# Optimization experiments

Hardware: AMD Instinct MI355X
Metric: run time of the kernel (lower is better)

## Reference

```python
import jax, jax.numpy as jnp
import numpy as np

DIM = 384
HEADS = 12
W = 7  # window_size
N = W * W
B = 4096

def _relative_position_index(ws):
    ch = np.arange(ws)
    coords = np.stack(np.meshgrid(ch, ch, indexing='ij'))  # [2, W, W]
    cf = coords.reshape(2, -1)  # [2, W*W]
    rel = cf[:, :, None] - cf[:, None, :]  # [2, N, N]
    rel = rel.transpose(1, 2, 0)
    rel[:, :, 0] += ws - 1
    rel[:, :, 1] += ws - 1
    rel[:, :, 0] *= 2 * ws - 1
    return rel.sum(-1).astype(np.int32)  # [N, N]

def setup_inputs() -> dict:
    key = jax.random.key(0)
    ks = jax.random.split(key, 8)
    s = 0.02
    return {
        'x': jax.random.normal(ks[0], (B, N, DIM), jnp.float32),
        'y': jax.random.normal(ks[1], (B, N, DIM), jnp.float32),
        'q_w': jax.random.normal(ks[2], (DIM, DIM), jnp.float32) * s,
        'q_b': jnp.zeros((DIM,), jnp.float32),
        'kv_w': jax.random.normal(ks[3], (2 * DIM, DIM), jnp.float32) * s,
        'kv_b': jnp.zeros((2 * DIM,), jnp.float32),
        'proj_w': jax.random.normal(ks[4], (DIM, DIM), jnp.float32) * s,
        'proj_b': jnp.zeros((DIM,), jnp.float32),
        'rel_table': jax.random.normal(ks[5], ((2 * W - 1) ** 2, HEADS), jnp.float32) * s,
        'rel_index': jnp.asarray(_relative_position_index(W)),
    }

def reference(x, y, q_w, q_b, kv_w, kv_b, proj_w, proj_b, rel_table, rel_index):
    Bx, N1, C = x.shape
    N2 = y.shape[1]
    hd = C // HEADS
    scale = hd ** -0.5
    # projections (torch Linear: x @ W^T + b)
    q = (x @ q_w.T + q_b).reshape(Bx, N1, HEADS, hd)
    kv = (y @ kv_w.T + kv_b).reshape(Bx, N2, 2, HEADS, hd)
    k = kv[:, :, 0]  # [B, N2, H, d]
    v = kv[:, :, 1]
    attn = jnp.einsum('bqhd,bkhd->bhqk', q, k) * scale
    # relative position bias: [N1, N2, H] -> [H, N1, N2]
    bias = rel_table[rel_index.reshape(-1)].reshape(N1, N2, HEADS)
    attn = attn + jnp.transpose(bias, (2, 0, 1))[None]
    attn = jax.nn.softmax(attn, axis=-1)
    out = jnp.einsum('bhqk,bkhd->bqhd', attn, v).reshape(Bx, N1, C)
    return out @ proj_w.T + proj_b
```

## Files before the change

### kernel.cpp

```cpp
#include <hip/hip_runtime.h>

#define DIM 384
#define HEADS 12
#define HD 32
#define NTOK 49
#define NWIN 4096
#define MTOT (NWIN*NTOK)
#define PSTR 72

typedef __attribute__((ext_vector_type(8))) __bf16 bf16x8;
typedef __attribute__((ext_vector_type(4))) __bf16 bf16x4;
typedef __attribute__((ext_vector_type(4))) float f32x4;

static __device__ __forceinline__ f32x4 mfma16(bf16x8 a, bf16x8 b, f32x4 c) {
  return __builtin_amdgcn_mfma_f32_16x16x32_bf16(a, b, c, 0, 0, 0);
}

static __device__ __forceinline__ void gload_lds16(const void* g, void* l) {
  __builtin_amdgcn_global_load_lds(
      (const __attribute__((address_space(1))) unsigned int*)g,
      (__attribute__((address_space(3))) unsigned int*)l, 16, 0, 0);
}

static __device__ __forceinline__ bf16x4 cvt4(float4 v) {
  bf16x4 t;
  t[0]=(__bf16)v.x; t[1]=(__bf16)v.y; t[2]=(__bf16)v.z; t[3]=(__bf16)v.w;
  return t;
}

__global__ void k_prep(const float* __restrict__ qw, const float* __restrict__ kvw,
                       const float* __restrict__ pw, const float* __restrict__ rel_table,
                       const int* __restrict__ rel_index,
                       __bf16* __restrict__ qw_bf, __bf16* __restrict__ kvw_bf,
                       __bf16* __restrict__ pw_bf, float* __restrict__ bias_pad) {
  int i = blockIdx.x * 256 + threadIdx.x;
  if (i < DIM*DIM)   qw_bf[i] = (__bf16)qw[i];
  if (i < 2*DIM*DIM) kvw_bf[i] = (__bf16)kvw[i];
  if (i < DIM*DIM)   pw_bf[i] = (__bf16)pw[i];
  if (i < HEADS*64*64) {
    int h = i >> 12, rem = i & 4095, q = rem >> 6, k = rem & 63;
    float v;
    if (k >= NTOK)      v = -1e30f;
    else if (q >= NTOK) v = 0.0f;
    else v = rel_table[rel_index[q*NTOK + k] * HEADS + h];
    bias_pad[i] = v;
  }
}

__global__ __launch_bounds__(256, 4) void k_qkv(
    const float* __restrict__ x, const float* __restrict__ y,
    const __bf16* __restrict__ qw_bf, const __bf16* __restrict__ kvw_bf,
    const float* __restrict__ q_b, const float* __restrict__ kv_b,
    __bf16* __restrict__ Qws, __bf16* __restrict__ Kws, __bf16* __restrict__ Vws)
{
  int b = blockIdx.x;
  int orig = (b & 7) * 1764 + (b >> 3);
  int mtile = orig / 9;
  int nt9 = orig - mtile*9;
  const float* A; const __bf16* Bw; const float* bias; __bf16* Cout;
  int wrow0, col0;
  if (nt9 < 3) { A = x; Bw = qw_bf; bias = q_b; Cout = Qws; wrow0 = nt9*128; col0 = wrow0; }
  else {
    A = y; Bw = kvw_bf; bias = kv_b; wrow0 = (nt9-3)*128;
    if (wrow0 < DIM) { Cout = Kws; col0 = wrow0; } else { Cout = Vws; col0 = wrow0 - DIM; }
  }
  bias += wrow0;

  __shared__ __align__(16) __bf16 As[2*128*32];
  __shared__ __align__(16) __bf16 Bs[3*128*32];

  int t = threadIdx.x, lane = t & 63, wave = t >> 6;
  int l15 = lane & 15, g = lane >> 4;
  int wr = (wave >> 1) * 64, wc = (wave & 1) * 64;
  int row0b = mtile*128;

  int c8 = lane & 7;
  int r8 = lane >> 3;
  int swk = (lane >> 4) & 3;
  const float* asrc = A + (size_t)(row0b + wave*32 + r8)*DIM + c8*4;
  unsigned lwb = (unsigned)wave*2048 + (unsigned)r8*64
               + ((((c8 >> 1) ^ swk) << 4) + (c8 & 1)*8);

  int sr  = 2*(lane >> 3) + ((lane >> 2) & 1);
  int scb = (lane & 3) ^ ((lane >> 3) & 3);
  const __bf16* bsrc0 = Bw + (size_t)(wrow0 + (wave*2    )*16 + sr)*DIM + scb*8;
  const __bf16* bsrc1 = Bw + (size_t)(wrow0 + (wave*2 + 1)*16 + sr)*DIM + scb*8;

  f32x4 acc[4][4];
  #pragma unroll
  for (int a=0;a<4;a++)
    #pragma unroll
    for (int bb=0;bb<4;bb++) acc[a][bb] = (f32x4){0.f,0.f,0.f,0.f};

  {
    float4 s0 = *(const float4*)(asrc);
    float4 s1 = *(const float4*)(asrc +  8*DIM);
    float4 s2 = *(const float4*)(asrc + 16*DIM);
    float4 s3 = *(const float4*)(asrc + 24*DIM);
    gload_lds16(bsrc0,      (char*)Bs +        (wave*2  )*1024);
    gload_lds16(bsrc1,      (char*)Bs +        (wave*2+1)*1024);
    gload_lds16(bsrc0 + 32, (char*)Bs + 8192 + (wave*2  )*1024);
    gload_lds16(bsrc1 + 32, (char*)Bs + 8192 + (wave*2+1)*1024);
    *(bf16x4*)((char*)As + lwb +    0) = cvt4(s0);
    *(bf16x4*)((char*)As + lwb +  512) = cvt4(s1);
    *(bf16x4*)((char*)As + lwb + 1024) = cvt4(s2);
    *(bf16x4*)((char*)As + lwb + 1536) = cvt4(s3);
    asm volatile("s_waitcnt vmcnt(2)" ::: "memory");
    asm volatile("s_waitcnt lgkmcnt(0)" ::: "memory");
    __builtin_amdgcn_s_barrier();
  }

  int lslot = l15*64 + ((g ^ ((l15 >> 1) & 3)) << 4);

  #pragma unroll
  for (int kt = 0; kt < 12; ++kt) {
    const int cur2 = kt & 1, nxt2 = cur2 ^ 1;
    const int cur3 = kt % 3, pre3 = (kt + 2) % 3;
    float4 s0, s1, s2, s3;
    if (kt < 11) {
      int kk = (kt + 1) * 32;
      s0 = *(const float4*)(asrc + kk);
      s1 = *(const float4*)(asrc + kk +  8*DIM);
      s2 = *(const float4*)(asrc + kk + 16*DIM);
      s3 = *(const float4*)(asrc + kk + 24*DIM);
    }
    if (kt < 10) {
      int kk = (kt + 2) * 32;
      gload_lds16(bsrc0 + kk, (char*)Bs + pre3*8192 + (wave*2  )*1024);
      gload_lds16(bsrc1 + kk, (char*)Bs + pre3*8192 + (wave*2+1)*1024);
    }
    bf16x8 af[4], bfv[4];
    #pragma unroll
    for (int a=0;a<4;a++)
      af[a]  = *(const bf16x8*)((const char*)As + cur2*8192 + (wr + a*16)*64 + lslot);
    #pragma unroll
    for (int bb=0;bb<4;bb++)
      bfv[bb] = *(const bf16x8*)((const char*)Bs + cur3*8192 + (wc + bb*16)*64 + lslot);
    #pragma unroll
    for (int a=0;a<4;a++)
      #pragma unroll
      for (int bb=0;bb<4;bb++)
        acc[a][bb] = mfma16(af[a], bfv[bb], acc[a][bb]);
    if (kt < 11) {
      *(bf16x4*)((char*)As + nxt2*8192 + lwb +    0) = cvt4(s0);
      *(bf16x4*)((char*)As + nxt2*8192 + lwb +  512) = cvt4(s1);
      *(bf16x4*)((char*)As + nxt2*8192 + lwb + 1024) = cvt4(s2);
      *(bf16x4*)((char*)As + nxt2*8192 + lwb + 1536) = cvt4(s3);
      if (kt < 10) asm volatile("s_waitcnt vmcnt(2)" ::: "memory");
      else         asm volatile("s_waitcnt vmcnt(0)" ::: "memory");
      asm volatile("s_waitcnt lgkmcnt(0)" ::: "memory");
      __builtin_amdgcn_s_barrier();
    }
  }

  #pragma unroll
  for (int a=0;a<4;a++) {
    #pragma unroll
    for (int bb=0;bb<4;bb++) {
      int colw = wc + bb*16 + l15;
      float bi = bias[colw];
      size_t cbase = (size_t)(row0b + wr + a*16 + 4*g)*DIM + (col0 + colw);
      #pragma unroll
      for (int r=0;r<4;r++)
        Cout[cbase + (size_t)r*DIM] = (__bf16)(acc[a][bb][r] + bi);
    }
  }
}

__global__ __launch_bounds__(256) void k_attn(
    __bf16* qao,
    const __bf16* __restrict__ Kws, const __bf16* __restrict__ Vws,
    const float* __restrict__ bias_pad)
{
  __shared__ __align__(16) __bf16 Psh[4][64*PSTR];
  __shared__ __align__(16) __bf16 VTsh[4][32*PSTR];
  int b = blockIdx.x;
  int lane = threadIdx.x & 63, wave = threadIdx.x >> 6;
  int l15 = lane & 15, g = lane >> 4;
  __bf16* Pw  = Psh[wave];
  __bf16* VTw = VTsh[wave];
  size_t rowbase = (size_t)b * NTOK * DIM;
  const float scale = 0.17677669529663687f;

  for (int e = lane; e < 32*15; e += 64) {
    int d = e / 15, k = 49 + (e - d*15);
    VTw[d*PSTR + k] = (__bf16)0.0f;
  }

  for (int hh = 0; hh < 3; hh++) {
    int h = wave + hh*4;
    for (int e = lane; e < NTOK*HD; e += 64) {
      int k = e >> 5, d = e & 31;
      VTw[d*PSTR + k] = Vws[rowbase + (size_t)k*DIM + h*HD + d];
    }
    bf16x8 qf[4], kf[4];
    #pragma unroll
    for (int mt=0; mt<4; mt++) {
      int q = 16*mt + l15; if (q > 48) q = 48;
      qf[mt] = *(const bf16x8*)(qao + rowbase + (size_t)q*DIM + h*HD + g*8);
    }
    #pragma unroll
    for (int nt=0; nt<4; nt++) {
      int kk = 16*nt + l15; if (kk > 48) kk = 48;
      kf[nt] = *(const bf16x8*)(Kws + rowbase + (size_t)kk*DIM + h*HD + g*8);
    }
    f32x4 sacc[4][4];
    #pragma unroll
    for (int mt=0; mt<4; mt++)
      #pragma unroll
      for (int nt=0; nt<4; nt++)
        sacc[mt][nt] = mfma16(qf[mt], kf[nt], (f32x4){0.f,0.f,0.f,0.f});

    const float* bt = bias_pad + h*4096;
    float rs[4][4];
    #pragma unroll
    for (int mt=0; mt<4; mt++) {
      #pragma unroll
      for (int r=0; r<4; r++) {
        int q = 16*mt + 4*g + r;
        float v0 = sacc[mt][0][r]*scale + bt[q*64 +  0 + l15];
        float v1 = sacc[mt][1][r]*scale + bt[q*64 + 16 + l15];
        float v2 = sacc[mt][2][r]*scale + bt[q*64 + 32 + l15];
        float v3 = sacc[mt][3][r]*scale + bt[q*64 + 48 + l15];
        float m = fmaxf(fmaxf(v0,v1), fmaxf(v2,v3));
        #pragma unroll
        for (int off=1; off<16; off<<=1) m = fmaxf(m, __shfl_xor(m, off));
        v0 = __expf(v0-m); v1 = __expf(v1-m); v2 = __expf(v2-m); v3 = __expf(v3-m);
        float s = v0+v1+v2+v3;
        #pragma unroll
        for (int off=1; off<16; off<<=1) s += __shfl_xor(s, off);
        rs[mt][r] = s;
        Pw[q*PSTR +  0 + l15] = (__bf16)v0;
        Pw[q*PSTR + 16 + l15] = (__bf16)v1;
        Pw[q*PSTR + 32 + l15] = (__bf16)v2;
        Pw[q*PSTR + 48 + l15] = (__bf16)v3;
      }
    }

    #pragma unroll
    for (int mt=0; mt<4; mt++) {
      #pragma unroll
      for (int dt=0; dt<2; dt++) {
        f32x4 o = (f32x4){0.f,0.f,0.f,0.f};
        #pragma unroll
        for (int ks=0; ks<2; ks++) {
          bf16x8 pa = *(const bf16x8*)(Pw  + (16*mt + l15)*PSTR + 32*ks + 8*g);
          bf16x8 vb = *(const bf16x8*)(VTw + (16*dt + l15)*PSTR + 32*ks + 8*g);
          o = mfma16(pa, vb, o);
        }
        #pragma unroll
        for (int r=0; r<4; r++) {
          int q = 16*mt + 4*g + r;
          if (q < NTOK)
            qao[rowbase + (size_t)q*DIM + h*HD + 16*dt + l15] = (__bf16)(o[r] / rs[mt][r]);
        }
      }
    }
  }
}

__global__ __launch_bounds__(256, 4) void k_proj(
    const __bf16* __restrict__ Aao, const __bf16* __restrict__ pw_bf,
    const float* __restrict__ pb, float* __restrict__ out)
{
  int b = blockIdx.x;
  int orig = (b & 7) * 588 + (b >> 3);
  int mtile = orig / 3;
  int nt = orig - mtile*3;
  int lane = threadIdx.x & 63, wave = threadIdx.x >> 6;
  int l15 = lane & 15, g = lane >> 4;
  int wr = (wave >> 1) * 64, wc = (wave & 1) * 64;
  int row0b = mtile*128;
  int col00 = nt*128;

  __shared__ __align__(16) __bf16 As[3*128*32];
  __shared__ __align__(16) __bf16 Bs[3*128*32];

  int sr  = 2*(lane >> 3) + ((lane >> 2) & 1);
  int scb = (lane & 3) ^ ((lane >> 3) & 3);
  const __bf16* asrc0 = Aao   + (size_t)(row0b + (wave*2    )*16 + sr)*DIM + scb*8;
  const __bf16* asrc1 = Aao   + (size_t)(row0b + (wave*2 + 1)*16 + sr)*DIM + scb*8;
  const __bf16* bsrc0 = pw_bf + (size_t)(col00 + (wave*2    )*16 + sr)*DIM + scb*8;
  const __bf16* bsrc1 = pw_bf + (size_t)(col00 + (wave*2 + 1)*16 + sr)*DIM + scb*8;

  f32x4 acc[4][4];
  #pragma unroll
  for (int a=0;a<4;a++)
    #pragma unroll
    for (int bb=0;bb<4;bb++) acc[a][bb] = (f32x4){0.f,0.f,0.f,0.f};

  {
    gload_lds16(asrc0,      (char*)As +        (wave*2  )*1024);
    gload_lds16(asrc1,      (char*)As +        (wave*2+1)*1024);
    gload_lds16(bsrc0,      (char*)Bs +        (wave*2  )*1024);
    gload_lds16(bsrc1,      (char*)Bs +        (wave*2+1)*1024);
    gload_lds16(asrc0 + 32, (char*)As + 8192 + (wave*2  )*1024);
    gload_lds16(asrc1 + 32, (char*)As + 8192 + (wave*2+1)*1024);
    gload_lds16(bsrc0 + 32, (char*)Bs + 8192 + (wave*2  )*1024);
    gload_lds16(bsrc1 + 32, (char*)Bs + 8192 + (wave*2+1)*1024);
    asm volatile("s_waitcnt vmcnt(4)" ::: "memory");
    __builtin_amdgcn_s_barrier();
  }

  int lslot = l15*64 + ((g ^ ((l15 >> 1) & 3)) << 4);

  #pragma unroll
  for (int kt = 0; kt < 12; ++kt) {
    const int cur3 = kt % 3, pre3 = (kt + 2) % 3;
    if (kt < 10) {
      int kk = (kt + 2) * 32;
      gload_lds16(asrc0 + kk, (char*)As + pre3*8192 + (wave*2  )*1024);
      gload_lds16(asrc1 + kk, (char*)As + pre3*8192 + (wave*2+1)*1024);
      gload_lds16(bsrc0 + kk, (char*)Bs + pre3*8192 + (wave*2  )*1024);
      gload_lds16(bsrc1 + kk, (char*)Bs + pre3*8192 + (wave*2+1)*1024);
    }
    bf16x8 af[4], bfv[4];
    #pragma unroll
    for (int a=0;a<4;a++)
      af[a]  = *(const bf16x8*)((const char*)As + cur3*8192 + (wr + a*16)*64 + lslot);
    #pragma unroll
    for (int bb=0;bb<4;bb++)
      bfv[bb] = *(const bf16x8*)((const char*)Bs + cur3*8192 + (wc + bb*16)*64 + lslot);
    #pragma unroll
    for (int a=0;a<4;a++)
      #pragma unroll
      for (int bb=0;bb<4;bb++)
        acc[a][bb] = mfma16(af[a], bfv[bb], acc[a][bb]);
    if (kt < 11) {
      if (kt < 10) asm volatile("s_waitcnt vmcnt(4)" ::: "memory");
      else         asm volatile("s_waitcnt vmcnt(0)" ::: "memory");
      __builtin_amdgcn_s_barrier();
    }
  }

  #pragma unroll
  for (int a=0;a<4;a++) {
    #pragma unroll
    for (int bb=0;bb<4;bb++) {
      int col = col00 + wc + bb*16 + l15;
      float bi = pb[col];
      size_t cbase = (size_t)(row0b + wr + a*16 + 4*g)*DIM + col;
      #pragma unroll
      for (int r=0;r<4;r++)
        out[cbase + (size_t)r*DIM] = acc[a][bb][r] + bi;
    }
  }
}

extern "C" void kernel_launch(void* const* d_in, const int* in_sizes, int n_in,
                              void* d_out, int out_size, void* d_ws, size_t ws_size,
                              hipStream_t stream)
{
  const float* x   = (const float*)d_in[0];
  const float* y   = (const float*)d_in[1];
  const float* qw  = (const float*)d_in[2];
  const float* qb  = (const float*)d_in[3];
  const float* kvw = (const float*)d_in[4];
  const float* kvb = (const float*)d_in[5];
  const float* pw  = (const float*)d_in[6];
  const float* pb  = (const float*)d_in[7];
  const float* rt  = (const float*)d_in[8];
  const int*   ri  = (const int*)d_in[9];
  float* out = (float*)d_out;

  char* ws = (char*)d_ws;
  const size_t WS_NEEDED = 1376256ull + 3ull*154140672ull;
  if (ws_size < WS_NEEDED) return;

  __bf16* qw_bf    = (__bf16*)(ws);
  __bf16* kvw_bf   = (__bf16*)(ws + 294912);
  __bf16* pw_bf    = (__bf16*)(ws + 884736);
  float*  bias_pad = (float*)(ws + 1179648);
  __bf16* Qws      = (__bf16*)(ws + 1376256);
  __bf16* Kws      = Qws + (size_t)MTOT*DIM;
  __bf16* Vws      = Kws + (size_t)MTOT*DIM;

  k_prep<<<dim3(1152), dim3(256), 0, stream>>>(qw, kvw, pw, rt, ri, qw_bf, kvw_bf, pw_bf, bias_pad);
  k_qkv <<<dim3(1568*9), dim3(256), 0, stream>>>(x, y, qw_bf, kvw_bf, qb, kvb, Qws, Kws, Vws);
  k_attn<<<dim3(NWIN), dim3(256), 0, stream>>>(Qws, Kws, Vws, bias_pad);
  k_proj<<<dim3(1568*3), dim3(256), 0, stream>>>(Qws, pw_bf, pb, out);
}
```

Before: 840.8 us.

## Keep full-K activation row panel in LDS and sweep all output columns

```diff
diff --git a/kernel.cpp b/kernel.cpp
--- a/kernel.cpp
+++ b/kernel.cpp
@@ -47,122 +47,111 @@
   }
 }
 
-__global__ __launch_bounds__(256, 4) void k_qkv(
+__global__ __launch_bounds__(256, 2) void k_qkv2(
     const float* __restrict__ x, const float* __restrict__ y,
     const __bf16* __restrict__ qw_bf, const __bf16* __restrict__ kvw_bf,
     const float* __restrict__ q_b, const float* __restrict__ kv_b,
     __bf16* __restrict__ Qws, __bf16* __restrict__ Kws, __bf16* __restrict__ Vws)
 {
-  int b = blockIdx.x;
-  int orig = (b & 7) * 1764 + (b >> 3);
-  int mtile = orig / 9;
-  int nt9 = orig - mtile*9;
-  const float* A; const __bf16* Bw; const float* bias; __bf16* Cout;
-  int wrow0, col0;
-  if (nt9 < 3) { A = x; Bw = qw_bf; bias = q_b; Cout = Qws; wrow0 = nt9*128; col0 = wrow0; }
-  else {
-    A = y; Bw = kvw_bf; bias = kv_b; wrow0 = (nt9-3)*128;
-    if (wrow0 < DIM) { Cout = Kws; col0 = wrow0; } else { Cout = Vws; col0 = wrow0 - DIM; }
-  }
-  bias += wrow0;
-
-  __shared__ __align__(16) __bf16 As[2*128*32];
+  __shared__ __align__(16) __bf16 Asub[12*64*32];
   __shared__ __align__(16) __bf16 Bs[3*128*32];
 
-  int t = threadIdx.x, lane = t & 63, wave = t >> 6;
-  int l15 = lane & 15, g = lane >> 4;
-  int wr = (wave >> 1) * 64, wc = (wave & 1) * 64;
-  int row0b = mtile*128;
-
-  int c8 = lane & 7;
-  int r8 = lane >> 3;
-  int swk = (lane >> 4) & 3;
-  const float* asrc = A + (size_t)(row0b + wave*32 + r8)*DIM + c8*4;
-  unsigned lwb = (unsigned)wave*2048 + (unsigned)r8*64
-               + ((((c8 >> 1) ^ swk) << 4) + (c8 & 1)*8);
-
-  int sr  = 2*(lane >> 3) + ((lane >> 2) & 1);
-  int scb = (lane & 3) ^ ((lane >> 3) & 3);
-  const __bf16* bsrc0 = Bw + (size_t)(wrow0 + (wave*2    )*16 + sr)*DIM + scb*8;
-  const __bf16* bsrc1 = Bw + (size_t)(wrow0 + (wave*2 + 1)*16 + sr)*DIM + scb*8;
-
-  f32x4 acc[4][4];
-  #pragma unroll
-  for (int a=0;a<4;a++)
-    #pragma unroll
-    for (int bb=0;bb<4;bb++) acc[a][bb] = (f32x4){0.f,0.f,0.f,0.f};
+  const int b = blockIdx.x;
+  const int type = b & 1;
+  const int mtile = b >> 1;
+  const float* A = type ? y : x;
+  const __bf16* Bw = type ? kvw_bf : qw_bf;
+  const int NCH = type ? 6 : 3;
+  const int row0b = mtile * 64;
+
+  const int t = threadIdx.x, lane = t & 63, wave = t >> 6;
+  const int l15 = lane & 15, g = lane >> 4;
+  const int wm = wave >> 1, wn = wave & 1;
 
   {
-    float4 s0 = *(const float4*)(asrc);
-    float4 s1 = *(const float4*)(asrc +  8*DIM);
-    float4 s2 = *(const float4*)(asrc + 16*DIM);
-    float4 s3 = *(const float4*)(asrc + 24*DIM);
-    gload_lds16(bsrc0,      (char*)Bs +        (wave*2  )*1024);
-    gload_lds16(bsrc1,      (char*)Bs +        (wave*2+1)*1024);
-    gload_lds16(bsrc0 + 32, (char*)Bs + 8192 + (wave*2  )*1024);
-    gload_lds16(bsrc1 + 32, (char*)Bs + 8192 + (wave*2+1)*1024);
-    *(bf16x4*)((char*)As + lwb +    0) = cvt4(s0);
-    *(bf16x4*)((char*)As + lwb +  512) = cvt4(s1);
-    *(bf16x4*)((char*)As + lwb + 1024) = cvt4(s2);
-    *(bf16x4*)((char*)As + lwb + 1536) = cvt4(s3);
-    asm volatile("s_waitcnt vmcnt(2)" ::: "memory");
-    asm volatile("s_waitcnt lgkmcnt(0)" ::: "memory");
-    __builtin_amdgcn_s_barrier();
-  }
-
-  int lslot = l15*64 + ((g ^ ((l15 >> 1) & 3)) << 4);
-
-  #pragma unroll
-  for (int kt = 0; kt < 12; ++kt) {
-    const int cur2 = kt & 1, nxt2 = cur2 ^ 1;
-    const int cur3 = kt % 3, pre3 = (kt + 2) % 3;
-    float4 s0, s1, s2, s3;
-    if (kt < 11) {
-      int kk = (kt + 1) * 32;
-      s0 = *(const float4*)(asrc + kk);
-      s1 = *(const float4*)(asrc + kk +  8*DIM);
-      s2 = *(const float4*)(asrc + kk + 16*DIM);
-      s3 = *(const float4*)(asrc + kk + 24*DIM);
-    }
-    if (kt < 10) {
-      int kk = (kt + 2) * 32;
-      gload_lds16(bsrc0 + kk, (char*)Bs + pre3*8192 + (wave*2  )*1024);
-      gload_lds16(bsrc1 + kk, (char*)Bs + pre3*8192 + (wave*2+1)*1024);
-    }
-    bf16x8 af[4], bfv[4];
-    #pragma unroll
-    for (int a=0;a<4;a++)
-      af[a]  = *(const bf16x8*)((const char*)As + cur2*8192 + (wr + a*16)*64 + lslot);
-    #pragma unroll
-    for (int bb=0;bb<4;bb++)
-      bfv[bb] = *(const bf16x8*)((const char*)Bs + cur3*8192 + (wc + bb*16)*64 + lslot);
-    #pragma unroll
-    for (int a=0;a<4;a++)
+    const int c8 = lane & 7, r8 = lane >> 3;
+    const int swk = (lane >> 4) & 3;
+    const float* asrc = A + (size_t)(row0b + wave*8 + r8)*DIM + c8*4;
+    const unsigned lwA = (unsigned)(wave*8 + r8)*64
+                       + ((((c8 >> 1) ^ swk) << 4) + (c8 & 1)*8);
+    #pragma unroll
+    for (int st = 0; st < 12; ++st) {
+      float4 u0 = *(const float4*)(asrc + st*32);
+      float4 u1 = *(const float4*)(asrc + st*32 + 32*DIM);
+      *(bf16x4*)((char*)Asub + st*4096 + lwA)        = cvt4(u0);
+      *(bf16x4*)((char*)Asub + st*4096 + 2048 + lwA) = cvt4(u1);
+    }
+  }
+
+  const int sr  = 2*(lane >> 3) + ((lane >> 2) & 1);
+  const int scb = (lane & 3) ^ ((lane >> 3) & 3);
+  const __bf16* bsrc0 = Bw + (size_t)((wave*2    )*16 + sr)*DIM + scb*8;
+  const __bf16* bsrc1 = Bw + (size_t)((wave*2 + 1)*16 + sr)*DIM + scb*8;
+
+  gload_lds16(bsrc0,      (char*)Bs        + (wave*2  )*1024);
+  gload_lds16(bsrc1,      (char*)Bs        + (wave*2+1)*1024);
+  gload_lds16(bsrc0 + 32, (char*)Bs + 8192 + (wave*2  )*1024);
+  gload_lds16(bsrc1 + 32, (char*)Bs + 8192 + (wave*2+1)*1024);
+  asm volatile("s_waitcnt lgkmcnt(0)" ::: "memory");
+  __builtin_amdgcn_s_barrier();
+
+  const int lslot = l15*64 + ((g ^ ((l15 >> 1) & 3)) << 4);
+
+  for (int jn = 0; jn < NCH; ++jn) {
+    const size_t co = (size_t)jn * 49152;
+    const size_t cn = co + 49152;
+    f32x4 acc[2][4];
+    #pragma unroll
+    for (int a=0;a<2;a++)
+      #pragma unroll
+      for (int bb=0;bb<4;bb++) acc[a][bb] = (f32x4){0.f,0.f,0.f,0.f};
+
+    #pragma unroll
+    for (int kt = 0; kt < 12; ++kt) {
+      if (kt == 11 && jn == NCH-1) asm volatile("s_waitcnt vmcnt(0)" ::: "memory");
+      else                         asm volatile("s_waitcnt vmcnt(2)" ::: "memory");
+      __builtin_amdgcn_s_barrier();
+
+      const int cb = kt % 3;
+      bf16x8 af[2], bfv[4];
+      af[0] = *(const bf16x8*)((const char*)Asub + kt*4096 + (wm*32     )*64 + lslot);
+      af[1] = *(const bf16x8*)((const char*)Asub + kt*4096 + (wm*32 + 16)*64 + lslot);
       #pragma unroll
       for (int bb=0;bb<4;bb++)
-        acc[a][bb] = mfma16(af[a], bfv[bb], acc[a][bb]);
-    if (kt < 11) {
-      *(bf16x4*)((char*)As + nxt2*8192 + lwb +    0) = cvt4(s0);
-      *(bf16x4*)((char*)As + nxt2*8192 + lwb +  512) = cvt4(s1);
-      *(bf16x4*)((char*)As + nxt2*8192 + lwb + 1024) = cvt4(s2);
-      *(bf16x4*)((char*)As + nxt2*8192 + lwb + 1536) = cvt4(s3);
-      if (kt < 10) asm volatile("s_waitcnt vmcnt(2)" ::: "memory");
-      else         asm volatile("s_waitcnt vmcnt(0)" ::: "memory");
-      asm volatile("s_waitcnt lgkmcnt(0)" ::: "memory");
-      __builtin_amdgcn_s_barrier();
-    }
-  }
-
-  #pragma unroll
-  for (int a=0;a<4;a++) {
-    #pragma unroll
-    for (int bb=0;bb<4;bb++) {
-      int colw = wc + bb*16 + l15;
-      float bi = bias[colw];
-      size_t cbase = (size_t)(row0b + wr + a*16 + 4*g)*DIM + (col0 + colw);
-      #pragma unroll
-      for (int r=0;r<4;r++)
-        Cout[cbase + (size_t)r*DIM] = (__bf16)(acc[a][bb][r] + bi);
+        bfv[bb] = *(const bf16x8*)((const char*)Bs + cb*8192 + (wn*64 + bb*16)*64 + lslot);
+
+      if (kt < 10) {
+        gload_lds16(bsrc0 + co + (kt+2)*32, (char*)Bs + ((kt+2)%3)*8192 + (wave*2  )*1024);
+        gload_lds16(bsrc1 + co + (kt+2)*32, (char*)Bs + ((kt+2)%3)*8192 + (wave*2+1)*1024);
+      } else if (jn < NCH-1) {
+        const int k2 = kt - 10;
+        gload_lds16(bsrc0 + cn + k2*32, (char*)Bs + ((kt+2)%3)*8192 + (wave*2  )*1024);
+        gload_lds16(bsrc1 + cn + k2*32, (char*)Bs + ((kt+2)%3)*8192 + (wave*2+1)*1024);
+      }
+
+      #pragma unroll
+      for (int a=0;a<2;a++)
+        #pragma unroll
+        for (int bb=0;bb<4;bb++)
+          acc[a][bb] = mfma16(af[a], bfv[bb], acc[a][bb]);
+    }
+
+    const float* biasp = (type ? kv_b : q_b) + jn*128;
+    __bf16* Cout; int col0;
+    if (!type)        { Cout = Qws; col0 = jn*128; }
+    else if (jn < 3)  { Cout = Kws; col0 = jn*128; }
+    else              { Cout = Vws; col0 = (jn-3)*128; }
+    #pragma unroll
+    for (int a=0;a<2;a++) {
+      #pragma unroll
+      for (int bb=0;bb<4;bb++) {
+        const int colw = wn*64 + bb*16 + l15;
+        const float bi = biasp[colw];
+        const size_t cbase = (size_t)(row0b + wm*32 + a*16 + 4*g)*DIM + col0 + colw;
+        #pragma unroll
+        for (int r=0;r<4;r++)
+          Cout[cbase + (size_t)r*DIM] = (__bf16)(acc[a][bb][r] + bi);
+      }
     }
   }
 }
@@ -259,90 +248,98 @@
   }
 }
 
-__global__ __launch_bounds__(256, 4) void k_proj(
+__global__ __launch_bounds__(256, 2) void k_proj2(
     const __bf16* __restrict__ Aao, const __bf16* __restrict__ pw_bf,
     const float* __restrict__ pb, float* __restrict__ out)
 {
-  int b = blockIdx.x;
-  int orig = (b & 7) * 588 + (b >> 3);
-  int mtile = orig / 3;
-  int nt = orig - mtile*3;
-  int lane = threadIdx.x & 63, wave = threadIdx.x >> 6;
-  int l15 = lane & 15, g = lane >> 4;
-  int wr = (wave >> 1) * 64, wc = (wave & 1) * 64;
-  int row0b = mtile*128;
-  int col00 = nt*128;
-
-  __shared__ __align__(16) __bf16 As[3*128*32];
+  __shared__ __align__(16) __bf16 Asub[12*64*32];
   __shared__ __align__(16) __bf16 Bs[3*128*32];
 
-  int sr  = 2*(lane >> 3) + ((lane >> 2) & 1);
-  int scb = (lane & 3) ^ ((lane >> 3) & 3);
-  const __bf16* asrc0 = Aao   + (size_t)(row0b + (wave*2    )*16 + sr)*DIM + scb*8;
-  const __bf16* asrc1 = Aao   + (size_t)(row0b + (wave*2 + 1)*16 + sr)*DIM + scb*8;
-  const __bf16* bsrc0 = pw_bf + (size_t)(col00 + (wave*2    )*16 + sr)*DIM + scb*8;
-  const __bf16* bsrc1 = pw_bf + (size_t)(col00 + (wave*2 + 1)*16 + sr)*DIM + scb*8;
-
-  f32x4 acc[4][4];
-  #pragma unroll
-  for (int a=0;a<4;a++)
-    #pragma unroll
-    for (int bb=0;bb<4;bb++) acc[a][bb] = (f32x4){0.f,0.f,0.f,0.f};
+  const int mtile = blockIdx.x;
+  const int row0b = mtile * 64;
+  const int t = threadIdx.x, lane = t & 63, wave = t >> 6;
+  const int l15 = lane & 15, g = lane >> 4;
+  const int wm = wave >> 1, wn = wave & 1;
+
+  const int sr  = 2*(lane >> 3) + ((lane >> 2) & 1);
+  const int scb = (lane & 3) ^ ((lane >> 3) & 3);
 
   {
-    gload_lds16(asrc0,      (char*)As +        (wave*2  )*1024);
-    gload_lds16(asrc1,      (char*)As +        (wave*2+1)*1024);
-    gload_lds16(bsrc0,      (char*)Bs +        (wave*2  )*1024);
-    gload_lds16(bsrc1,      (char*)Bs +        (wave*2+1)*1024);
-    gload_lds16(asrc0 + 32, (char*)As + 8192 + (wave*2  )*1024);
-    gload_lds16(asrc1 + 32, (char*)As + 8192 + (wave*2+1)*1024);
-    gload_lds16(bsrc0 + 32, (char*)Bs + 8192 + (wave*2  )*1024);
-    gload_lds16(bsrc1 + 32, (char*)Bs + 8192 + (wave*2+1)*1024);
-    asm volatile("s_waitcnt vmcnt(4)" ::: "memory");
-    __builtin_amdgcn_s_barrier();
-  }
-
-  int lslot = l15*64 + ((g ^ ((l15 >> 1) & 3)) << 4);
-
-  #pragma unroll
-  for (int kt = 0; kt < 12; ++kt) {
-    const int cur3 = kt % 3, pre3 = (kt + 2) % 3;
-    if (kt < 10) {
-      int kk = (kt + 2) * 32;
-      gload_lds16(asrc0 + kk, (char*)As + pre3*8192 + (wave*2  )*1024);
-      gload_lds16(asrc1 + kk, (char*)As + pre3*8192 + (wave*2+1)*1024);
-      gload_lds16(bsrc0 + kk, (char*)Bs + pre3*8192 + (wave*2  )*1024);
-      gload_lds16(bsrc1 + kk, (char*)Bs + pre3*8192 + (wave*2+1)*1024);
-    }
-    bf16x8 af[4], bfv[4];
-    #pragma unroll
-    for (int a=0;a<4;a++)
-      af[a]  = *(const bf16x8*)((const char*)As + cur3*8192 + (wr + a*16)*64 + lslot);
-    #pragma unroll
-    for (int bb=0;bb<4;bb++)
-      bfv[bb] = *(const bf16x8*)((const char*)Bs + cur3*8192 + (wc + bb*16)*64 + lslot);
-    #pragma unroll
-    for (int a=0;a<4;a++)
+    const __bf16* aj0 = Aao + (size_t)(row0b +  0 + sr)*DIM + scb*8;
+    const __bf16* aj1 = Aao + (size_t)(row0b + 16 + sr)*DIM + scb*8;
+    const __bf16* aj2 = Aao + (size_t)(row0b + 32 + sr)*DIM + scb*8;
+    const __bf16* aj3 = Aao + (size_t)(row0b + 48 + sr)*DIM + scb*8;
+    #pragma unroll
+    for (int stl = 0; stl < 3; ++stl) {
+      const int st = wave*3 + stl;
+      gload_lds16(aj0 + st*32, (char*)Asub + st*4096 +    0);
+      gload_lds16(aj1 + st*32, (char*)Asub + st*4096 + 1024);
+      gload_lds16(aj2 + st*32, (char*)Asub + st*4096 + 2048);
+      gload_lds16(aj3 + st*32, (char*)Asub + st*4096 + 3072);
+    }
+  }
+
+  const __bf16* bsrc0 = pw_bf + (size_t)((wave*2    )*16 + sr)*DIM + scb*8;
+  const __bf16* bsrc1 = pw_bf + (size_t)((wave*2 + 1)*16 + sr)*DIM + scb*8;
+  gload_lds16(bsrc0,      (char*)Bs        + (wave*2  )*1024);
+  gload_lds16(bsrc1,      (char*)Bs        + (wave*2+1)*1024);
+  gload_lds16(bsrc0 + 32, (char*)Bs + 8192 + (wave*2  )*1024);
+  gload_lds16(bsrc1 + 32, (char*)Bs + 8192 + (wave*2+1)*1024);
+  asm volatile("s_waitcnt vmcnt(4)" ::: "memory");
+  __builtin_amdgcn_s_barrier();
+
+  const int lslot = l15*64 + ((g ^ ((l15 >> 1) & 3)) << 4);
+
+  for (int jn = 0; jn < 3; ++jn) {
+    const size_t co = (size_t)jn * 49152;
+    const size_t cn = co + 49152;
+    f32x4 acc[2][4];
+    #pragma unroll
+    for (int a=0;a<2;a++)
+      #pragma unroll
+      for (int bb=0;bb<4;bb++) acc[a][bb] = (f32x4){0.f,0.f,0.f,0.f};
+
+    #pragma unroll
+    for (int kt = 0; kt < 12; ++kt) {
+      if (kt == 11 && jn == 2) asm volatile("s_waitcnt vmcnt(0)" ::: "memory");
+      else                     asm volatile("s_waitcnt vmcnt(2)" ::: "memory");
+      __builtin_amdgcn_s_barrier();
+
+      const int cb = kt % 3;
+      bf16x8 af[2], bfv[4];
+      af[0] = *(const bf16x8*)((const char*)Asub + kt*4096 + (wm*32     )*64 + lslot);
+      af[1] = *(const bf16x8*)((const char*)Asub + kt*4096 + (wm*32 + 16)*64 + lslot);
       #pragma unroll
       for (int bb=0;bb<4;bb++)
-        acc[a][bb] = mfma16(af[a], bfv[bb], acc[a][bb]);
-    if (kt < 11) {
-      if (kt < 10) asm volatile("s_waitcnt vmcnt(4)" ::: "memory");
-      else         asm volatile("s_waitcnt vmcnt(0)" ::: "memory");
-      __builtin_amdgcn_s_barrier();
-    }
-  }
-
-  #pragma unroll
-  for (int a=0;a<4;a++) {
-    #pragma unroll
-    for (int bb=0;bb<4;bb++) {
-      int col = col00 + wc + bb*16 + l15;
-      float bi = pb[col];
-      size_t cbase = (size_t)(row0b + wr + a*16 + 4*g)*DIM + col;
-      #pragma unroll
-      for (int r=0;r<4;r++)
-        out[cbase + (size_t)r*DIM] = acc[a][bb][r] + bi;
+        bfv[bb] = *(const bf16x8*)((const char*)Bs + cb*8192 + (wn*64 + bb*16)*64 + lslot);
+
+      if (kt < 10) {
+        gload_lds16(bsrc0 + co + (kt+2)*32, (char*)Bs + ((kt+2)%3)*8192 + (wave*2  )*1024);
+        gload_lds16(bsrc1 + co + (kt+2)*32, (char*)Bs + ((kt+2)%3)*8192 + (wave*2+1)*1024);
+      } else if (jn < 2) {
+        const int k2 = kt - 10;
+        gload_lds16(bsrc0 + cn + k2*32, (char*)Bs + ((kt+2)%3)*8192 + (wave*2  )*1024);
+        gload_lds16(bsrc1 + cn + k2*32, (char*)Bs + ((kt+2)%3)*8192 + (wave*2+1)*1024);
+      }
+
+      #pragma unroll
+      for (int a=0;a<2;a++)
+        #pragma unroll
+        for (int bb=0;bb<4;bb++)
+          acc[a][bb] = mfma16(af[a], bfv[bb], acc[a][bb]);
+    }
+
+    #pragma unroll
+    for (int a=0;a<2;a++) {
+      #pragma unroll
+      for (int bb=0;bb<4;bb++) {
+        const int col = jn*128 + wn*64 + bb*16 + l15;
+        const float bi = pb[col];
+        const size_t cbase = (size_t)(row0b + wm*32 + a*16 + 4*g)*DIM + col;
+        #pragma unroll
+        for (int r=0;r<4;r++)
+          out[cbase + (size_t)r*DIM] = acc[a][bb][r] + bi;
+      }
     }
   }
 }
@@ -375,8 +372,8 @@
   __bf16* Kws      = Qws + (size_t)MTOT*DIM;
   __bf16* Vws      = Kws + (size_t)MTOT*DIM;
 
-  k_prep<<<dim3(1152), dim3(256), 0, stream>>>(qw, kvw, pw, rt, ri, qw_bf, kvw_bf, pw_bf, bias_pad);
-  k_qkv <<<dim3(1568*9), dim3(256), 0, stream>>>(x, y, qw_bf, kvw_bf, qb, kvb, Qws, Kws, Vws);
-  k_attn<<<dim3(NWIN), dim3(256), 0, stream>>>(Qws, Kws, Vws, bias_pad);
-  k_proj<<<dim3(1568*3), dim3(256), 0, stream>>>(Qws, pw_bf, pb, out);
-}
+  k_prep <<<dim3(1152), dim3(256), 0, stream>>>(qw, kvw, pw, rt, ri, qw_bf, kvw_bf, pw_bf, bias_pad);
+  k_qkv2 <<<dim3(2*3136), dim3(256), 0, stream>>>(x, y, qw_bf, kvw_bf, qb, kvb, Qws, Kws, Vws);
+  k_attn <<<dim3(NWIN), dim3(256), 0, stream>>>(Qws, Kws, Vws, bias_pad);
+  k_proj2<<<dim3(3136), dim3(256), 0, stream>>>(Qws, pw_bf, pb, out);
+}
```

Result: slower. 901.3 us (+7.2%).

## Split attention into one-wave blocks and fold softmax scale into Q projection

Applied to the files above, without the earlier changes.

```diff
diff --git a/kernel.cpp b/kernel.cpp
--- a/kernel.cpp
+++ b/kernel.cpp
@@ -65,6 +65,7 @@
     if (wrow0 < DIM) { Cout = Kws; col0 = wrow0; } else { Cout = Vws; col0 = wrow0 - DIM; }
   }
   bias += wrow0;
+  const float osc = (nt9 < 3) ? 0.17677669529663687f : 1.0f;
 
   __shared__ __align__(16) __bf16 As[2*128*32];
   __shared__ __align__(16) __bf16 Bs[3*128*32];
@@ -162,25 +163,24 @@
       size_t cbase = (size_t)(row0b + wr + a*16 + 4*g)*DIM + (col0 + colw);
       #pragma unroll
       for (int r=0;r<4;r++)
-        Cout[cbase + (size_t)r*DIM] = (__bf16)(acc[a][bb][r] + bi);
-    }
-  }
-}
-
-__global__ __launch_bounds__(256) void k_attn(
+        Cout[cbase + (size_t)r*DIM] = (__bf16)((acc[a][bb][r] + bi) * osc);
+    }
+  }
+}
+
+__global__ __launch_bounds__(64) void k_attn(
     __bf16* qao,
     const __bf16* __restrict__ Kws, const __bf16* __restrict__ Vws,
     const float* __restrict__ bias_pad)
 {
-  __shared__ __align__(16) __bf16 Psh[4][64*PSTR];
-  __shared__ __align__(16) __bf16 VTsh[4][32*PSTR];
-  int b = blockIdx.x;
-  int lane = threadIdx.x & 63, wave = threadIdx.x >> 6;
+  __shared__ __align__(16) __bf16 Pw[64*PSTR];
+  __shared__ __align__(16) __bf16 VTw[32*PSTR];
+  int bid = blockIdx.x;
+  int b = bid >> 2;
+  int hq = bid & 3;
+  int lane = threadIdx.x;
   int l15 = lane & 15, g = lane >> 4;
-  __bf16* Pw  = Psh[wave];
-  __bf16* VTw = VTsh[wave];
   size_t rowbase = (size_t)b * NTOK * DIM;
-  const float scale = 0.17677669529663687f;
 
   for (int e = lane; e < 32*15; e += 64) {
     int d = e / 15, k = 49 + (e - d*15);
@@ -188,7 +188,7 @@
   }
 
   for (int hh = 0; hh < 3; hh++) {
-    int h = wave + hh*4;
+    int h = hq + hh*4;
     for (int e = lane; e < NTOK*HD; e += 64) {
       int k = e >> 5, d = e & 31;
       VTw[d*PSTR + k] = Vws[rowbase + (size_t)k*DIM + h*HD + d];
@@ -218,10 +218,10 @@
       #pragma unroll
       for (int r=0; r<4; r++) {
         int q = 16*mt + 4*g + r;
-        float v0 = sacc[mt][0][r]*scale + bt[q*64 +  0 + l15];
-        float v1 = sacc[mt][1][r]*scale + bt[q*64 + 16 + l15];
-        float v2 = sacc[mt][2][r]*scale + bt[q*64 + 32 + l15];
-        float v3 = sacc[mt][3][r]*scale + bt[q*64 + 48 + l15];
+        float v0 = sacc[mt][0][r] + bt[q*64 +  0 + l15];
+        float v1 = sacc[mt][1][r] + bt[q*64 + 16 + l15];
+        float v2 = sacc[mt][2][r] + bt[q*64 + 32 + l15];
+        float v3 = sacc[mt][3][r] + bt[q*64 + 48 + l15];
         float m = fmaxf(fmaxf(v0,v1), fmaxf(v2,v3));
         #pragma unroll
         for (int off=1; off<16; off<<=1) m = fmaxf(m, __shfl_xor(m, off));
@@ -229,7 +229,7 @@
         float s = v0+v1+v2+v3;
         #pragma unroll
         for (int off=1; off<16; off<<=1) s += __shfl_xor(s, off);
-        rs[mt][r] = s;
+        rs[mt][r] = __frcp_rn(s);
         Pw[q*PSTR +  0 + l15] = (__bf16)v0;
         Pw[q*PSTR + 16 + l15] = (__bf16)v1;
         Pw[q*PSTR + 32 + l15] = (__bf16)v2;
@@ -252,7 +252,7 @@
         for (int r=0; r<4; r++) {
           int q = 16*mt + 4*g + r;
           if (q < NTOK)
-            qao[rowbase + (size_t)q*DIM + h*HD + 16*dt + l15] = (__bf16)(o[r] / rs[mt][r]);
+            qao[rowbase + (size_t)q*DIM + h*HD + 16*dt + l15] = (__bf16)(o[r] * rs[mt][r]);
         }
       }
     }
@@ -377,6 +377,6 @@
 
   k_prep<<<dim3(1152), dim3(256), 0, stream>>>(qw, kvw, pw, rt, ri, qw_bf, kvw_bf, pw_bf, bias_pad);
   k_qkv <<<dim3(1568*9), dim3(256), 0, stream>>>(x, y, qw_bf, kvw_bf, qb, kvb, Qws, Kws, Vws);
-  k_attn<<<dim3(NWIN), dim3(256), 0, stream>>>(Qws, Kws, Vws, bias_pad);
+  k_attn<<<dim3(NWIN*4), dim3(64), 0, stream>>>(Qws, Kws, Vws, bias_pad);
   k_proj<<<dim3(1568*3), dim3(256), 0, stream>>>(Qws, pw_bf, pb, out);
 }
```

Measured after the change: 865.8 us. 1.03x slower.
